# Kernel tuning notes

Measured on AMD Instinct MI355X. Metric: run time of the kernel, lower is better.

The kernel has to match this reference:

```python
import jax, jax.numpy as jnp
import numpy as np

B, D, C = 4096, 4096, 1024


def setup_inputs() -> dict:
    key = jax.random.key(0)
    kx, kw = jax.random.split(key)
    x = jax.random.normal(kx, (B, D), dtype=jnp.float32)
    # kaiming_normal_ with nonlinearity='relu': std = sqrt(2 / fan_in)
    W = jax.random.normal(kw, (C, D), dtype=jnp.float32) * jnp.sqrt(2.0 / D)
    return {"x": x, "W": W}


def reference(x, W):
    # Original: -( (x[:, :, None] - W.T[None, :, :])**2 ).mean(axis=1)
    d = x.shape[1]
    x_sq = jnp.sum(x * x, axis=1, keepdims=True)        # [B, 1]
    w_sq = jnp.sum(W * W, axis=1)[None, :]              # [1, C]
    cross = jnp.einsum('bd,cd->bc', x, W)               # [B, C] tensor-core GEMM
    return -(x_sq - 2.0 * cross + w_sq) / d
```

## Files before the change

kernel.cpp:

```cpp
#include <hip/hip_runtime.h>
#include <hip/hip_bf16.h>


typedef float f32x4 __attribute__((ext_vector_type(4)));
typedef unsigned short ushort4_t __attribute__((ext_vector_type(4)));
typedef long long2_t __attribute__((ext_vector_type(2)));

#define BDIM 4096
#define DDIM 4096
#define CDIM 1024
#define TM 128
#define TN 128
#define BK 64
#define KSPLIT 4
#define NIT ((DDIM / KSPLIT) / BK)
#define SCALE 32.0f
#define INV_SS (1.0f/1024.0f)

#define SYNC_LGKM() asm volatile("s_waitcnt lgkmcnt(0)\n\ts_barrier" ::: "memory")

__device__ __forceinline__ unsigned short f2bf(float f) {
    unsigned int u = __float_as_uint(f);
    unsigned int rounding = 0x7FFFu + ((u >> 16) & 1u);
    return (unsigned short)((u + rounding) >> 16);
}

__global__ __launch_bounds__(256) void cvt_rowsq(
    const float* __restrict__ x, const float* __restrict__ W,
    unsigned char* __restrict__ xb, unsigned char* __restrict__ wb,
    float* __restrict__ xsq, float* __restrict__ wsq)
{
    const int lane = threadIdx.x & 63;
    const int row = blockIdx.x * 4 + (threadIdx.x >> 6);

    const float* src;
    unsigned char* dst;
    float* sq;
    if (row < BDIM) {
        src = x + (size_t)row * DDIM;
        dst = xb + (size_t)row * DDIM;
        sq = xsq + row;
    } else {
        int r = row - BDIM;
        src = W + (size_t)r * DDIM;
        dst = wb + (size_t)r * DDIM;
        sq = wsq + r;
    }

    const float4* s4 = (const float4*)src;
    unsigned int* d4 = (unsigned int*)dst;
    float a = 0.f;
    #pragma unroll
    for (int s = 0; s < DDIM / 4 / 64; ++s) {
        float4 f = s4[lane + 64 * s];
        a += f.x * f.x + f.y * f.y + f.z * f.z + f.w * f.w;
        unsigned int p = 0;
        p = __builtin_amdgcn_cvt_pk_fp8_f32(f.x * SCALE, f.y * SCALE, p, false);
        p = __builtin_amdgcn_cvt_pk_fp8_f32(f.z * SCALE, f.w * SCALE, p, true);
        d4[lane + 64 * s] = p;
    }
    #pragma unroll
    for (int off = 32; off > 0; off >>= 1) a += __shfl_down(a, off);
    if (lane == 0) *sq = a;
}

struct Pref { long2_t a0, a1, b0, b1; };

__global__ __launch_bounds__(256, 3) void gemm_eucl(
    const unsigned char* __restrict__ xb,
    const unsigned char* __restrict__ wb,
    unsigned short* __restrict__ part)
{
    __shared__ unsigned char sm[2 * 16384];

    const int tid = threadIdx.x;
    const int lane = tid & 63;
    const int wid = tid >> 6;
    const int bm = blockIdx.x * TM;
    const int bn = blockIdx.y * TN;
    const int ks = blockIdx.z * (DDIM / KSPLIT);
    const int wm = (wid >> 1) * 64;
    const int wn = (wid & 1) * 64;

    const int r0 = tid >> 2, c = tid & 3;
    const unsigned char* gA0 = xb + (size_t)(bm + r0) * DDIM + ks + c * 16;
    const unsigned char* gA1 = gA0 + (size_t)64 * DDIM;
    const unsigned char* gB0 = wb + (size_t)(bn + r0) * DDIM + ks + c * 16;
    const unsigned char* gB1 = gB0 + (size_t)64 * DDIM;

    const int k2o = (c >> 1) * 8;
    const int kcw = (c & 1) * 2;
    const int wo0 = r0 * 64 + ((kcw ^ (r0 & 3)) * 16) + k2o;
    const int wo1 = r0 * 64 + (((kcw | 1) ^ (r0 & 3)) * 16) + k2o;

    const int kc = lane >> 4;
    const int ml = lane & 15;
    int aoff[4], boff[4];
    #pragma unroll
    for (int i = 0; i < 4; ++i) {
        int m = wm + i * 16 + ml;
        aoff[i] = m * 64 + ((kc ^ (m & 3)) * 16);
        int n = wn + i * 16 + ml;
        boff[i] = n * 64 + ((kc ^ (n & 3)) * 16);
    }

    f32x4 acc[4][4] = {};

#define LOADSET(S)                                                      \
    do {                                                                \
        (S).a0 = *(const long2_t*)gA0; (S).a1 = *(const long2_t*)gA1;   \
        (S).b0 = *(const long2_t*)gB0; (S).b1 = *(const long2_t*)gB1;   \
        gA0 += BK; gA1 += BK; gB0 += BK; gB1 += BK;                     \
    } while (0)

#define WRITESET(buf, S)                                                \
    do {                                                                \
        unsigned char* sA = sm + (buf) * 16384;                         \
        unsigned char* sB = sA + 8192;                                  \
        *(long*)(sA + wo0) = (S).a0.x; *(long*)(sA + wo1) = (S).a0.y;   \
        *(long*)(sA + wo0 + 4096) = (S).a1.x;                           \
        *(long*)(sA + wo1 + 4096) = (S).a1.y;                           \
        *(long*)(sB + wo0) = (S).b0.x; *(long*)(sB + wo1) = (S).b0.y;   \
        *(long*)(sB + wo0 + 4096) = (S).b1.x;                           \
        *(long*)(sB + wo1 + 4096) = (S).b1.y;                           \
    } while (0)

#define COMPUTE(buf)                                                    \
    do {                                                                \
        const unsigned char* sA = sm + (buf) * 16384;                   \
        const unsigned char* sB = sA + 8192;                            \
        long2_t la[4], lb[4];                                           \
        _Pragma("unroll")                                               \
        for (int i = 0; i < 4; ++i) la[i] = *(const long2_t*)(sA + aoff[i]); \
        _Pragma("unroll")                                               \
        for (int j = 0; j < 4; ++j) lb[j] = *(const long2_t*)(sB + boff[j]); \
        _Pragma("unroll")                                               \
        for (int i = 0; i < 4; ++i)                                     \
            _Pragma("unroll")                                           \
            for (int j = 0; j < 4; ++j) {                               \
                acc[i][j] = __builtin_amdgcn_mfma_f32_16x16x32_fp8_fp8( \
                    la[i].x, lb[j].x, acc[i][j], 0, 0, 0);              \
                acc[i][j] = __builtin_amdgcn_mfma_f32_16x16x32_fp8_fp8( \
                    la[i].y, lb[j].y, acc[i][j], 0, 0, 0);              \
            }                                                           \
    } while (0)

    Pref S0, S1;
    LOADSET(S0);
    LOADSET(S1);
    WRITESET(0, S0);
    SYNC_LGKM();

    #pragma unroll 1
    for (int kk = 0; kk < (NIT - 2) / 2; ++kk) {
        LOADSET(S0);
        COMPUTE(0);
        WRITESET(1, S1);
        SYNC_LGKM();
        LOADSET(S1);
        COMPUTE(1);
        WRITESET(0, S0);
        SYNC_LGKM();
    }
    COMPUTE(0);
    WRITESET(1, S1);
    SYNC_LGKM();
    COMPUTE(1);

    unsigned short* p = part + (size_t)blockIdx.z * BDIM * CDIM
                      + (size_t)(blockIdx.x * 8 + blockIdx.y) * 16384;
    #pragma unroll
    for (int i = 0; i < 4; ++i)
        #pragma unroll
        for (int j = 0; j < 4; ++j) {
            ushort4_t v;
            v[0] = f2bf(acc[i][j][0]); v[1] = f2bf(acc[i][j][1]);
            v[2] = f2bf(acc[i][j][2]); v[3] = f2bf(acc[i][j][3]);
            *(ushort4_t*)&p[(i * 4 + j) * 1024 + tid * 4] = v;
        }
#undef LOADSET
#undef WRITESET
#undef COMPUTE
}

__global__ __launch_bounds__(256) void reduce_out(
    const unsigned short* __restrict__ part, const float* __restrict__ xsq,
    const float* __restrict__ wsq, float* __restrict__ out)
{
    const int bb = blockIdx.x;
    const int t = threadIdx.x;
    const int lane = t & 63;
    const int wid = t >> 6;
    const int bm = (bb >> 3) * TM, bn = (bb & 7) * TN;
    const int wm = (wid >> 1) * 64, wn = (wid & 1) * 64;
    const int row_l = (lane >> 4) * 4, col_l = lane & 15;
    const size_t sl = (size_t)BDIM * CDIM;
    const float c1 = 2.0f * INV_SS / (float)DDIM;
    const float c2 = 1.0f / (float)DDIM;

    #pragma unroll
    for (int f = 0; f < 16; ++f) {
        size_t o = (size_t)bb * 16384 + f * 1024 + t * 4;
        ushort4_t p0 = *(const ushort4_t*)&part[o];
        ushort4_t p1 = *(const ushort4_t*)&part[o + sl];
        ushort4_t p2 = *(const ushort4_t*)&part[o + 2 * sl];
        ushort4_t p3 = *(const ushort4_t*)&part[o + 3 * sl];
        int i = f >> 2, j = f & 3;
        int gn = bn + wn + j * 16 + col_l;
        float wv = wsq[gn];
        #pragma unroll
        for (int r = 0; r < 4; ++r) {
            float s = __uint_as_float((unsigned int)p0[r] << 16)
                    + __uint_as_float((unsigned int)p1[r] << 16)
                    + __uint_as_float((unsigned int)p2[r] << 16)
                    + __uint_as_float((unsigned int)p3[r] << 16);
            int gm = bm + wm + i * 16 + row_l + r;
            out[(size_t)gm * CDIM + gn] = s * c1 - (xsq[gm] + wv) * c2;
        }
    }
}

__global__ void fallback_kernel(const float* __restrict__ x, const float* __restrict__ W,
                                float* __restrict__ out)
{
    int c = blockIdx.x * blockDim.x + threadIdx.x;
    int b = blockIdx.y;
    if (c >= CDIM) return;
    const float* xr = x + (size_t)b * DDIM;
    const float* wr = W + (size_t)c * DDIM;
    float xs = 0.f, ws = 0.f, cr = 0.f;
    for (int d = 0; d < DDIM; ++d) {
        float xv = xr[d], wv = wr[d];
        xs += xv * xv; ws += wv * wv; cr += xv * wv;
    }
    out[(size_t)b * CDIM + c] = (2.0f * cr - xs - ws) / (float)DDIM;
}

extern "C" void kernel_launch(void* const* d_in, const int* in_sizes, int n_in,
                              void* d_out, int out_size, void* d_ws, size_t ws_size,
                              hipStream_t stream) {
    const float* x = (const float*)d_in[0];
    const float* W = (const float*)d_in[1];
    float* out = (float*)d_out;

    size_t need = (size_t)(BDIM + CDIM) * DDIM
                + (size_t)(BDIM + CDIM) * sizeof(float)
                + (size_t)KSPLIT * BDIM * CDIM * 2;
    if (ws_size < need) {
        fallback_kernel<<<dim3(CDIM / 256, BDIM), 256, 0, stream>>>(x, W, out);
        return;
    }

    unsigned char* xb = (unsigned char*)d_ws;
    unsigned char* wb = xb + (size_t)BDIM * DDIM;
    float* xsq = (float*)(wb + (size_t)CDIM * DDIM);
    float* wsq = xsq + BDIM;
    unsigned short* part = (unsigned short*)(wsq + CDIM);

    cvt_rowsq<<<(BDIM + CDIM) / 4, 256, 0, stream>>>(x, W, xb, wb, xsq, wsq);
    gemm_eucl<<<dim3(BDIM / TM, CDIM / TN, KSPLIT), 256, 0, stream>>>(xb, wb, part);
    reduce_out<<<256, 256, 0, stream>>>(part, xsq, wsq, out);
}
```

Before: 146.9 us.

## Store split-K partials as fp8, deepen global prefetch, stagger A-fragment loads

Split-K partial sums are now packed to fp8 after a 1/16 scale instead of bf16, which halves the partial-sum write and read traffic between the GEMM and the reduction kernel. The GEMM main loop is fully unrolled with three register prefetch sets and 32-bit offsets. A-fragment LDS reads are interleaved with the MFMAs. The reduce kernel runs twice as many blocks. Quantizing partials to fp8 adds sizable rounding error and risks saturation, so accuracy may fall outside tolerance.

```diff
diff --git a/kernel.cpp b/kernel.cpp
--- a/kernel.cpp
+++ b/kernel.cpp
@@ -3,7 +3,7 @@
 
 
 typedef float f32x4 __attribute__((ext_vector_type(4)));
-typedef unsigned short ushort4_t __attribute__((ext_vector_type(4)));
+typedef float f32x2 __attribute__((ext_vector_type(2)));
 typedef long long2_t __attribute__((ext_vector_type(2)));
 
 #define BDIM 4096
@@ -16,14 +16,9 @@
 #define NIT ((DDIM / KSPLIT) / BK)
 #define SCALE 32.0f
 #define INV_SS (1.0f/1024.0f)
+#define PSCALE 0.0625f
 
 #define SYNC_LGKM() asm volatile("s_waitcnt lgkmcnt(0)\n\ts_barrier" ::: "memory")
-
-__device__ __forceinline__ unsigned short f2bf(float f) {
-    unsigned int u = __float_as_uint(f);
-    unsigned int rounding = 0x7FFFu + ((u >> 16) & 1u);
-    return (unsigned short)((u + rounding) >> 16);
-}
 
 __global__ __launch_bounds__(256) void cvt_rowsq(
     const float* __restrict__ x, const float* __restrict__ W,
@@ -69,7 +64,7 @@
 __global__ __launch_bounds__(256, 3) void gemm_eucl(
     const unsigned char* __restrict__ xb,
     const unsigned char* __restrict__ wb,
-    unsigned short* __restrict__ part)
+    unsigned int* __restrict__ part)
 {
     __shared__ unsigned char sm[2 * 16384];
 
@@ -83,10 +78,10 @@
     const int wn = (wid & 1) * 64;
 
     const int r0 = tid >> 2, c = tid & 3;
-    const unsigned char* gA0 = xb + (size_t)(bm + r0) * DDIM + ks + c * 16;
-    const unsigned char* gA1 = gA0 + (size_t)64 * DDIM;
-    const unsigned char* gB0 = wb + (size_t)(bn + r0) * DDIM + ks + c * 16;
-    const unsigned char* gB1 = gB0 + (size_t)64 * DDIM;
+    const unsigned int oA0 = (unsigned int)((bm + r0) * DDIM + ks + c * 16);
+    const unsigned int oA1 = oA0 + 64u * DDIM;
+    const unsigned int oB0 = (unsigned int)((bn + r0) * DDIM + ks + c * 16);
+    const unsigned int oB1 = oB0 + 64u * DDIM;
 
     const int k2o = (c >> 1) * 8;
     const int kcw = (c & 1) * 2;
@@ -106,116 +101,124 @@
 
     f32x4 acc[4][4] = {};
 
-#define LOADSET(S)                                                      \
-    do {                                                                \
-        (S).a0 = *(const long2_t*)gA0; (S).a1 = *(const long2_t*)gA1;   \
-        (S).b0 = *(const long2_t*)gB0; (S).b1 = *(const long2_t*)gB1;   \
-        gA0 += BK; gA1 += BK; gB0 += BK; gB1 += BK;                     \
-    } while (0)
-
-#define WRITESET(buf, S)                                                \
-    do {                                                                \
-        unsigned char* sA = sm + (buf) * 16384;                         \
-        unsigned char* sB = sA + 8192;                                  \
-        *(long*)(sA + wo0) = (S).a0.x; *(long*)(sA + wo1) = (S).a0.y;   \
-        *(long*)(sA + wo0 + 4096) = (S).a1.x;                           \
-        *(long*)(sA + wo1 + 4096) = (S).a1.y;                           \
-        *(long*)(sB + wo0) = (S).b0.x; *(long*)(sB + wo1) = (S).b0.y;   \
-        *(long*)(sB + wo0 + 4096) = (S).b1.x;                           \
-        *(long*)(sB + wo1 + 4096) = (S).b1.y;                           \
-    } while (0)
-
-#define COMPUTE(buf)                                                    \
-    do {                                                                \
-        const unsigned char* sA = sm + (buf) * 16384;                   \
-        const unsigned char* sB = sA + 8192;                            \
-        long2_t la[4], lb[4];                                           \
-        _Pragma("unroll")                                               \
-        for (int i = 0; i < 4; ++i) la[i] = *(const long2_t*)(sA + aoff[i]); \
-        _Pragma("unroll")                                               \
+#define LOADSET(S, KT)                                                   \
+    do {                                                                 \
+        (S).a0 = *(const long2_t*)(xb + oA0 + (KT) * BK);                \
+        (S).a1 = *(const long2_t*)(xb + oA1 + (KT) * BK);                \
+        (S).b0 = *(const long2_t*)(wb + oB0 + (KT) * BK);                \
+        (S).b1 = *(const long2_t*)(wb + oB1 + (KT) * BK);                \
+    } while (0)
+
+#define WRITESET(buf, S)                                                 \
+    do {                                                                 \
+        unsigned char* sA = sm + (buf) * 16384;                          \
+        unsigned char* sB = sA + 8192;                                   \
+        *(long*)(sA + wo0) = (S).a0.x; *(long*)(sA + wo1) = (S).a0.y;    \
+        *(long*)(sA + wo0 + 4096) = (S).a1.x;                            \
+        *(long*)(sA + wo1 + 4096) = (S).a1.y;                            \
+        *(long*)(sB + wo0) = (S).b0.x; *(long*)(sB + wo1) = (S).b0.y;    \
+        *(long*)(sB + wo0 + 4096) = (S).b1.x;                            \
+        *(long*)(sB + wo1 + 4096) = (S).b1.y;                            \
+    } while (0)
+
+#define MFMA8(LA, I)                                                     \
+    do {                                                                 \
+        _Pragma("unroll")                                                \
+        for (int j = 0; j < 4; ++j) {                                    \
+            acc[I][j] = __builtin_amdgcn_mfma_f32_16x16x32_fp8_fp8(      \
+                (LA).x, lb[j].x, acc[I][j], 0, 0, 0);                    \
+            acc[I][j] = __builtin_amdgcn_mfma_f32_16x16x32_fp8_fp8(      \
+                (LA).y, lb[j].y, acc[I][j], 0, 0, 0);                    \
+        }                                                                \
+    } while (0)
+
+#define COMPUTE(buf)                                                     \
+    do {                                                                 \
+        const unsigned char* sA = sm + (buf) * 16384;                    \
+        const unsigned char* sB = sA + 8192;                             \
+        long2_t lb[4];                                                   \
+        _Pragma("unroll")                                                \
         for (int j = 0; j < 4; ++j) lb[j] = *(const long2_t*)(sB + boff[j]); \
-        _Pragma("unroll")                                               \
-        for (int i = 0; i < 4; ++i)                                     \
-            _Pragma("unroll")                                           \
-            for (int j = 0; j < 4; ++j) {                               \
-                acc[i][j] = __builtin_amdgcn_mfma_f32_16x16x32_fp8_fp8( \
-                    la[i].x, lb[j].x, acc[i][j], 0, 0, 0);              \
-                acc[i][j] = __builtin_amdgcn_mfma_f32_16x16x32_fp8_fp8( \
-                    la[i].y, lb[j].y, acc[i][j], 0, 0, 0);              \
-            }                                                           \
-    } while (0)
-
-    Pref S0, S1;
-    LOADSET(S0);
-    LOADSET(S1);
-    WRITESET(0, S0);
+        long2_t laA = *(const long2_t*)(sA + aoff[0]);                   \
+        long2_t laB = *(const long2_t*)(sA + aoff[1]);                   \
+        MFMA8(laA, 0);                                                   \
+        laA = *(const long2_t*)(sA + aoff[2]);                           \
+        MFMA8(laB, 1);                                                   \
+        laB = *(const long2_t*)(sA + aoff[3]);                           \
+        MFMA8(laA, 2);                                                   \
+        MFMA8(laB, 3);                                                   \
+    } while (0)
+
+    Pref S[3];
+    LOADSET(S[0], 0);
+    LOADSET(S[1], 1);
+    LOADSET(S[2], 2);
+    WRITESET(0, S[0]);
     SYNC_LGKM();
 
-    #pragma unroll 1
-    for (int kk = 0; kk < (NIT - 2) / 2; ++kk) {
-        LOADSET(S0);
-        COMPUTE(0);
-        WRITESET(1, S1);
+    #pragma unroll
+    for (int k = 0; k < NIT - 1; ++k) {
+        if (k < NIT - 3) LOADSET(S[k % 3], k + 3);
+        COMPUTE(k & 1);
+        WRITESET((k + 1) & 1, S[(k + 1) % 3]);
         SYNC_LGKM();
-        LOADSET(S1);
-        COMPUTE(1);
-        WRITESET(0, S0);
-        SYNC_LGKM();
-    }
-    COMPUTE(0);
-    WRITESET(1, S1);
-    SYNC_LGKM();
-    COMPUTE(1);
-
-    unsigned short* p = part + (size_t)blockIdx.z * BDIM * CDIM
-                      + (size_t)(blockIdx.x * 8 + blockIdx.y) * 16384;
+    }
+    COMPUTE((NIT - 1) & 1);
+
+    unsigned int* p = part
+        + (((size_t)blockIdx.z * 256 + (blockIdx.x * 8 + blockIdx.y)) * 16) * 256;
     #pragma unroll
     for (int i = 0; i < 4; ++i)
         #pragma unroll
         for (int j = 0; j < 4; ++j) {
-            ushort4_t v;
-            v[0] = f2bf(acc[i][j][0]); v[1] = f2bf(acc[i][j][1]);
-            v[2] = f2bf(acc[i][j][2]); v[3] = f2bf(acc[i][j][3]);
-            *(ushort4_t*)&p[(i * 4 + j) * 1024 + tid * 4] = v;
+            unsigned int pk = 0;
+            pk = __builtin_amdgcn_cvt_pk_fp8_f32(
+                acc[i][j][0] * PSCALE, acc[i][j][1] * PSCALE, pk, false);
+            pk = __builtin_amdgcn_cvt_pk_fp8_f32(
+                acc[i][j][2] * PSCALE, acc[i][j][3] * PSCALE, pk, true);
+            p[(i * 4 + j) * 256 + tid] = pk;
         }
 #undef LOADSET
 #undef WRITESET
+#undef MFMA8
 #undef COMPUTE
 }
 
 __global__ __launch_bounds__(256) void reduce_out(
-    const unsigned short* __restrict__ part, const float* __restrict__ xsq,
+    const unsigned int* __restrict__ part, const float* __restrict__ xsq,
     const float* __restrict__ wsq, float* __restrict__ out)
 {
-    const int bb = blockIdx.x;
+    const int bid = blockIdx.x;
+    const int bb = bid >> 1;
+    const int f0 = (bid & 1) * 8;
     const int t = threadIdx.x;
     const int lane = t & 63;
     const int wid = t >> 6;
     const int bm = (bb >> 3) * TM, bn = (bb & 7) * TN;
     const int wm = (wid >> 1) * 64, wn = (wid & 1) * 64;
     const int row_l = (lane >> 4) * 4, col_l = lane & 15;
-    const size_t sl = (size_t)BDIM * CDIM;
-    const float c1 = 2.0f * INV_SS / (float)DDIM;
+    const size_t sl = (size_t)256 * 16 * 256;
+    const float c1 = 2.0f * 16.0f * INV_SS / (float)DDIM;
     const float c2 = 1.0f / (float)DDIM;
 
     #pragma unroll
-    for (int f = 0; f < 16; ++f) {
-        size_t o = (size_t)bb * 16384 + f * 1024 + t * 4;
-        ushort4_t p0 = *(const ushort4_t*)&part[o];
-        ushort4_t p1 = *(const ushort4_t*)&part[o + sl];
-        ushort4_t p2 = *(const ushort4_t*)&part[o + 2 * sl];
-        ushort4_t p3 = *(const ushort4_t*)&part[o + 3 * sl];
+    for (int f = f0; f < f0 + 8; ++f) {
+        size_t o = ((size_t)bb * 16 + f) * 256 + t;
+        f32x2 s01 = {0.f, 0.f}, s23 = {0.f, 0.f};
+        #pragma unroll
+        for (int z = 0; z < KSPLIT; ++z) {
+            unsigned int u = part[o + (size_t)z * sl];
+            s01 += __builtin_amdgcn_cvt_pk_f32_fp8(u, false);
+            s23 += __builtin_amdgcn_cvt_pk_f32_fp8(u, true);
+        }
         int i = f >> 2, j = f & 3;
         int gn = bn + wn + j * 16 + col_l;
         float wv = wsq[gn];
+        float sv[4] = {s01.x, s01.y, s23.x, s23.y};
         #pragma unroll
         for (int r = 0; r < 4; ++r) {
-            float s = __uint_as_float((unsigned int)p0[r] << 16)
-                    + __uint_as_float((unsigned int)p1[r] << 16)
-                    + __uint_as_float((unsigned int)p2[r] << 16)
-                    + __uint_as_float((unsigned int)p3[r] << 16);
             int gm = bm + wm + i * 16 + row_l + r;
-            out[(size_t)gm * CDIM + gn] = s * c1 - (xsq[gm] + wv) * c2;
+            out[(size_t)gm * CDIM + gn] = sv[r] * c1 - (xsq[gm] + wv) * c2;
         }
     }
 }
@@ -245,7 +248,7 @@
 
     size_t need = (size_t)(BDIM + CDIM) * DDIM
                 + (size_t)(BDIM + CDIM) * sizeof(float)
-                + (size_t)KSPLIT * BDIM * CDIM * 2;
+                + (size_t)KSPLIT * BDIM * CDIM;
     if (ws_size < need) {
         fallback_kernel<<<dim3(CDIM / 256, BDIM), 256, 0, stream>>>(x, W, out);
         return;
@@ -255,9 +258,9 @@
     unsigned char* wb = xb + (size_t)BDIM * DDIM;
     float* xsq = (float*)(wb + (size_t)CDIM * DDIM);
     float* wsq = xsq + BDIM;
-    unsigned short* part = (unsigned short*)(wsq + CDIM);
+    unsigned int* part = (unsigned int*)(wsq + CDIM);
 
     cvt_rowsq<<<(BDIM + CDIM) / 4, 256, 0, stream>>>(x, W, xb, wb, xsq, wsq);
     gemm_eucl<<<dim3(BDIM / TM, CDIM / TN, KSPLIT), 256, 0, stream>>>(xb, wb, part);
-    reduce_out<<<256, 256, 0, stream>>>(part, xsq, wsq, out);
-}
+    reduce_out<<<512, 256, 0, stream>>>(part, xsq, wsq, out);
+}
```

Result: faster. 142.3 us (-3.1%).
